# Kernel tuning notes

Measured on AMD Instinct MI355X. Metric: run time of the kernel, lower is better.

Reference implementation:

```python
import jax, jax.numpy as jnp
import numpy as np

B, D, H, T = 16384, 64, 256, 64  # batch, state dim, ODE hidden, time steps
SH = 64  # SAC hidden dim


def setup_inputs() -> dict:
    key = jax.random.key(0)
    ks = jax.random.split(key, 24)
    inv = lambda n: 1.0 / np.sqrt(n)

    def mk(k, shape, scale):
        return jax.random.normal(k, shape, dtype=jnp.float32) * scale

    d = {}
    d["y0"] = jax.random.normal(ks[0], (B, D), dtype=jnp.float32)
    d["t"] = jnp.arange(T, dtype=jnp.float32)
    # pre-sampled standard-normal noise for Normal.rsample at each Euler step
    d["noise"] = jax.random.normal(ks[1], (T - 1, B, D), dtype=jnp.float32)
    # ODEFunc: Linear(D,H)+Tanh, Linear(H,H)+Softplus, Linear(H,D)  (num_layers=2)
    d["ode_W1"] = mk(ks[2], (D, H), inv(D));   d["ode_b1"] = mk(ks[3], (H,), 0.01)
    d["ode_W2"] = mk(ks[4], (H, H), inv(H));   d["ode_b2"] = mk(ks[5], (H,), 0.01)
    d["ode_W3"] = mk(ks[6], (H, D), 0.02);     d["ode_b3"] = mk(ks[7], (D,), 0.01)
    # SAC actor_mean: Linear(D,SH)+ReLU, Linear(SH,SH)+ReLU, Linear(SH,D)+Tanh
    d["am_W1"] = mk(ks[8], (D, SH), inv(D));   d["am_b1"] = mk(ks[9], (SH,), 0.01)
    d["am_W2"] = mk(ks[10], (SH, SH), inv(SH)); d["am_b2"] = mk(ks[11], (SH,), 0.01)
    d["am_W3"] = mk(ks[12], (SH, D), inv(SH)); d["am_b3"] = mk(ks[13], (D,), 0.01)
    # SAC actor_log_std: same shapes, no final tanh
    d["as_W1"] = mk(ks[14], (D, SH), inv(D));  d["as_b1"] = mk(ks[15], (SH,), 0.01)
    d["as_W2"] = mk(ks[16], (SH, SH), inv(SH)); d["as_b2"] = mk(ks[17], (SH,), 0.01)
    d["as_W3"] = mk(ks[18], (SH, D), inv(SH)); d["as_b3"] = mk(ks[19], (D,), 0.01)
    return d


def reference(y0, t, noise,
              ode_W1, ode_b1, ode_W2, ode_b2, ode_W3, ode_b3,
              am_W1, am_b1, am_W2, am_b2, am_W3, am_b3,
              as_W1, as_b1, as_W2, as_b2, as_W3, as_b3):
    dt = t[1] - t[0]  # source computes dt once from first interval

    def ode_func(y):  # ODEFunc.forward (t unused)
        h = jnp.tanh(y @ ode_W1 + ode_b1)
        h = jax.nn.softplus(h @ ode_W2 + ode_b2)
        return h @ ode_W3 + ode_b3

    def clean(x):  # where(isnan|isinf, 0, x)
        return jnp.where(jnp.isfinite(x), x, jnp.zeros_like(x))

    def actor_action(y, eps):  # SAC_Manifold action (critic unused by ODE forward)
        h = jax.nn.relu(y @ am_W1 + am_b1)
        h = jax.nn.relu(h @ am_W2 + am_b2)
        mean = clean(jnp.tanh(h @ am_W3 + am_b3))
        g = jax.nn.relu(y @ as_W1 + as_b1)
        g = jax.nn.relu(g @ as_W2 + as_b2)
        log_std = clean(g @ as_W3 + as_b3)
        std = jax.nn.softplus(log_std)
        x_t = mean + std * eps  # Normal.rsample
        return jnp.tanh(x_t)

    def step(y, eps):
        u = actor_action(y, eps)
        y_new = y + (ode_func(y) - u) * dt
        return y_new, y_new

    _, ys = jax.lax.scan(step, y0, noise)  # [T-1, B, D]
    return jnp.concatenate([y0[None], ys], axis=0)  # [T, B, D]
```

## Files before the change

kernel.cpp:

```cpp
#include <hip/hip_runtime.h>
#include <hip/hip_bf16.h>
#include <math.h>

#define NB 16384
#define DD 64
#define HH 256
#define NSTEP 63
#define RB 32
#define NT 512

#define SYW 68
#define SHW 260

#define O1H 0
#define O1L 16384
#define O2H 32768
#define O2L 98304
#define O3H 163840
#define O3L 180224
#define AM1H 196608
#define AM1L 200704
#define AM2H 204800
#define AM2L 208896
#define AM3H 212992
#define AM3L 217088
#define AS1H 221184
#define AS1L 225280
#define AS2H 229376
#define AS2L 233472
#define AS3H 237568
#define AS3L 241664
#define WB_SHORTS 245760

__device__ unsigned short g_wb[WB_SHORTS];

typedef __attribute__((ext_vector_type(8))) short s8v;
typedef __attribute__((ext_vector_type(4))) float f4v;
typedef __attribute__((ext_vector_type(4))) unsigned int u4v;

#define MFMA(a, b, c) __builtin_amdgcn_mfma_f32_16x16x32_bf16((a), (b), (c), 0, 0, 0)
#define MM3(acc, ah, al, bh, bl)                                 \
    do {                                                         \
        acc = MFMA(ah, bh, acc);                                 \
        acc = MFMA(ah, bl, acc);                                 \
        acc = MFMA(al, bh, acc);                                 \
    } while (0)

__device__ __forceinline__ unsigned short f2b(float x) {
    return __builtin_bit_cast(unsigned short, (__bf16)x);
}
__device__ __forceinline__ float b2f(unsigned short u) {
    return __builtin_bit_cast(float, (unsigned int)u << 16);
}
__device__ __forceinline__ unsigned int packsplit(float x) {
    const unsigned int xb = __builtin_bit_cast(unsigned int, x);
    const unsigned int hb = xb & 0xFFFF0000u;
    const float lof = x - __builtin_bit_cast(float, hb);
    const unsigned int lb = __builtin_bit_cast(unsigned int, lof);
    return __builtin_amdgcn_perm(lb, hb, 0x07060302);
}
__device__ __forceinline__ float fast_tanh(float x) {
    float e = __expf(-2.0f * fabsf(x));
    float r = __fdividef(1.0f - e, 1.0f + e);
    return copysignf(r, x);
}
__device__ __forceinline__ float fast_softplus(float x) {
    return fmaxf(x, 0.0f) + __logf(1.0f + __expf(-fabsf(x)));
}
__device__ __forceinline__ float clean_f(float x) { return isfinite(x) ? x : 0.0f; }
__device__ __forceinline__ f4v splat4(float b) { f4v v = {b, b, b, b}; return v; }

__device__ __forceinline__ void ldsPK(const unsigned int* p, s8v* hi, s8v* lo) {
    const u4v q0 = *(const u4v*)p;
    const u4v q1 = *(const u4v*)(p + 4);
    union { unsigned int u[4]; s8v v; } H, L;
    H.u[0] = __builtin_amdgcn_perm(q0[1], q0[0], 0x05040100);
    L.u[0] = __builtin_amdgcn_perm(q0[1], q0[0], 0x07060302);
    H.u[1] = __builtin_amdgcn_perm(q0[3], q0[2], 0x05040100);
    L.u[1] = __builtin_amdgcn_perm(q0[3], q0[2], 0x07060302);
    H.u[2] = __builtin_amdgcn_perm(q1[1], q1[0], 0x05040100);
    L.u[2] = __builtin_amdgcn_perm(q1[1], q1[0], 0x07060302);
    H.u[3] = __builtin_amdgcn_perm(q1[3], q1[2], 0x05040100);
    L.u[3] = __builtin_amdgcn_perm(q1[3], q1[2], 0x07060302);
    *hi = H.v; *lo = L.v;
}

__device__ __forceinline__ void gld16(const unsigned short* g, unsigned int* l) {
    __builtin_amdgcn_global_load_lds(
        (const __attribute__((address_space(1))) void*)(g),
        (__attribute__((address_space(3))) void*)(l), 16, 0, 0);
}

__device__ __forceinline__ s8v ldw(const unsigned int* wb, int j, int l) {
    return *(const s8v*)((const unsigned short*)wb + j * 512 + l * 8);
}

template <int C>
__device__ __forceinline__ void stage_chunk(unsigned int* dst, int w, int l) {
#pragma unroll
    for (int i = 0; i < 4; ++i) {
        const int j = w * 4 + i;
        int src;
        if constexpr (C == 0)
            src = 384 + ((j >> 4) * 48) + (((j >> 3) & 1) * 8) + (j & 7);
        else if constexpr (C == 1)
            src = 400 + ((j >> 4) * 48) + (((j >> 3) & 1) * 8) + (j & 7);
        else if constexpr (C == 2)
            src = 416 + ((j >> 4) * 48) + (((j >> 3) & 1) * 8) + (j & 7);
        else if constexpr (C == 3)
            src = (j & 15) * 2 + ((j >> 4) * 32);
        else if constexpr (C == 4)
            src = (j & 15) * 2 + 1 + ((j >> 4) * 32);
        else if constexpr (C >= 5 && C <= 12)
            src = 64 + ((j >> 4) * 128) + ((j & 15) * 8) + (C - 5);
        else if constexpr (C == 13)
            src = 320 + (((j >> 2) & 1) * 32) + ((j & 3) * 8) + (j >> 3);
        else
            src = 320 + (((j >> 2) & 1) * 32) + ((j & 3) * 8) + (j >> 3) + 4;
        gld16(g_wb + (size_t)src * 512 + l * 8, dst + j * 256);
    }
}

__global__ void prep_kernel(const float* __restrict__ W, int K, int N,
                            int hi_off, int lo_off) {
    const int l = threadIdx.x;
    const int kcN = K >> 5;
    const int nt = blockIdx.x / kcN;
    const int kc = blockIdx.x % kcN;
    const int col = nt * 16 + (l & 15);
    const int k0 = kc * 32 + ((l >> 4) << 3);
    const size_t base = ((size_t)(nt * kcN + kc) * 64 + l) * 8;
#pragma unroll
    for (int b = 0; b < 8; ++b) {
        float wv = W[(size_t)(k0 + b) * N + col];
        unsigned short h = f2b(wv);
        g_wb[hi_off + base + b] = h;
        g_wb[lo_off + base + b] = f2b(wv - b2f(h));
    }
}

#define SWAP_WB() do { unsigned int* _t = wc; wc = wn_; wn_ = _t; } while (0)

extern "C" __global__ void __launch_bounds__(NT)
ode_sac_kernel(const float* __restrict__ y0,
               const float* __restrict__ tarr,
               const float* __restrict__ noise,
               const float* __restrict__ ob1, const float* __restrict__ ob2,
               const float* __restrict__ ob3,
               const float* __restrict__ amb1, const float* __restrict__ amb2,
               const float* __restrict__ amb3,
               const float* __restrict__ asb1, const float* __restrict__ asb2,
               const float* __restrict__ asb3,
               float* __restrict__ out) {
    __shared__ __align__(16) unsigned int y_pk[RB * SYW];
    __shared__ __align__(16) unsigned int h1_pk[RB * SHW];
    __shared__ __align__(16) unsigned int h2_pk[RB * SHW];
    __shared__ __align__(16) unsigned int wbA[8192];
    __shared__ __align__(16) unsigned int wbB[8192];
    unsigned int* a1m = h1_pk;
    unsigned int* a1s = h1_pk + RB * SYW;
    unsigned int* a2m = h2_pk;
    unsigned int* a2s = h2_pk + RB * SYW;

    const int tid = threadIdx.x;
    const int w  = tid >> 6;
    const int l  = tid & 63;
    const int lm = l & 15;
    const int lg = l >> 4;
    const int wm = w >> 2;
    const int wn = w & 3;
    const int row0 = blockIdx.x * RB;
    const int cN = wn * 16 + lm;

    const float dt = tarr[1] - tarr[0];

    const float b_am1 = amb1[cN], b_am2 = amb2[cN], b_am3 = amb3[cN];
    const float b_as1 = asb1[cN], b_as2 = asb2[cN], b_as3 = asb3[cN];
    const float b_o3  = ob3[cN];
    const float b_o2a = ob2[(w * 2) * 16 + lm];
    const float b_o2b = ob2[(w * 2 + 1) * 16 + lm];
    float b_o1v[4];
#pragma unroll
    for (int nt = 0; nt < 4; ++nt) b_o1v[nt] = ob1[wn * 64 + nt * 16 + lm];

    stage_chunk<0>(wbA, w, l);
    float ysr[4];
#pragma unroll
    for (int r = 0; r < 4; ++r) {
        const int row = wm * 16 + lg * 4 + r;
        const float v = y0[(size_t)(row0 + row) * DD + cN];
        ysr[r] = v;
        y_pk[row * SYW + cN] = packsplit(v);
        __builtin_nontemporal_store(v, &out[(size_t)(row0 + row) * DD + cN]);
    }
    __syncthreads();
    unsigned int* wc = wbA;
    unsigned int* wn_ = wbB;

    for (int t = 0; t < NSTEP; ++t) {
        float u[4], ep[4];
        f4v accB[4];
        f4v acc4[2][2];
        f4v f3;

        stage_chunk<1>(wn_, w, l);
#pragma unroll
        for (int r = 0; r < 4; ++r) {
            const int row = wm * 16 + lg * 4 + r;
            ep[r] = __builtin_nontemporal_load(
                &noise[(size_t)t * NB * DD + (size_t)(row0 + row) * DD + cN]);
        }
        {
            f4v am = splat4(b_am1), as_ = splat4(b_as1);
#pragma unroll
            for (int kc = 0; kc < 2; ++kc) {
                s8v yh, yl;
                ldsPK(&y_pk[(wm * 16 + lm) * SYW + kc * 32 + lg * 8], &yh, &yl);
                MM3(am, yh, yl, ldw(wc, 2 * wn + kc, l), ldw(wc, 8 + 2 * wn + kc, l));
                MM3(as_, yh, yl, ldw(wc, 16 + 2 * wn + kc, l), ldw(wc, 24 + 2 * wn + kc, l));
            }
#pragma unroll
            for (int r = 0; r < 4; ++r) {
                const int row = wm * 16 + lg * 4 + r;
                a1m[row * SYW + cN] = packsplit(fmaxf(am[r], 0.0f));
                a1s[row * SYW + cN] = packsplit(fmaxf(as_[r], 0.0f));
            }
        }
        __syncthreads(); SWAP_WB();

        stage_chunk<2>(wn_, w, l);
        {
            f4v am = splat4(b_am2), as_ = splat4(b_as2);
#pragma unroll
            for (int kc = 0; kc < 2; ++kc) {
                const int k0 = kc * 32 + lg * 8;
                s8v mh, ml, sh, sl;
                ldsPK(&a1m[(wm * 16 + lm) * SYW + k0], &mh, &ml);
                ldsPK(&a1s[(wm * 16 + lm) * SYW + k0], &sh, &sl);
                MM3(am, mh, ml, ldw(wc, 2 * wn + kc, l), ldw(wc, 8 + 2 * wn + kc, l));
                MM3(as_, sh, sl, ldw(wc, 16 + 2 * wn + kc, l), ldw(wc, 24 + 2 * wn + kc, l));
            }
#pragma unroll
            for (int r = 0; r < 4; ++r) {
                const int row = wm * 16 + lg * 4 + r;
                a2m[row * SYW + cN] = packsplit(fmaxf(am[r], 0.0f));
                a2s[row * SYW + cN] = packsplit(fmaxf(as_[r], 0.0f));
            }
        }
        __syncthreads(); SWAP_WB();

        stage_chunk<3>(wn_, w, l);
        {
            f4v m3 = splat4(b_am3), s3 = splat4(b_as3);
#pragma unroll
            for (int kc = 0; kc < 2; ++kc) {
                const int k0 = kc * 32 + lg * 8;
                s8v mh, ml, sh, sl;
                ldsPK(&a2m[(wm * 16 + lm) * SYW + k0], &mh, &ml);
                ldsPK(&a2s[(wm * 16 + lm) * SYW + k0], &sh, &sl);
                MM3(m3, mh, ml, ldw(wc, 2 * wn + kc, l), ldw(wc, 8 + 2 * wn + kc, l));
                MM3(s3, sh, sl, ldw(wc, 16 + 2 * wn + kc, l), ldw(wc, 24 + 2 * wn + kc, l));
            }
#pragma unroll
            for (int r = 0; r < 4; ++r) {
                const float mean = clean_f(fast_tanh(m3[r]));
                const float ls   = clean_f(s3[r]);
                const float sd   = fast_softplus(ls);
                u[r] = fast_tanh(mean + sd * ep[r]);
            }
        }
        __syncthreads(); SWAP_WB();

        stage_chunk<4>(wn_, w, l);
        {
#pragma unroll
            for (int nt = 0; nt < 4; ++nt) accB[nt] = splat4(b_o1v[nt]);
            s8v yh, yl;
            ldsPK(&y_pk[(wm * 16 + lm) * SYW + 0 * 32 + lg * 8], &yh, &yl);
#pragma unroll
            for (int nt = 0; nt < 4; ++nt)
                MM3(accB[nt], yh, yl, ldw(wc, 4 * wn + nt, l), ldw(wc, 16 + 4 * wn + nt, l));
        }
        __syncthreads(); SWAP_WB();

        stage_chunk<5>(wn_, w, l);
        {
            s8v yh, yl;
            ldsPK(&y_pk[(wm * 16 + lm) * SYW + 1 * 32 + lg * 8], &yh, &yl);
#pragma unroll
            for (int nt = 0; nt < 4; ++nt)
                MM3(accB[nt], yh, yl, ldw(wc, 4 * wn + nt, l), ldw(wc, 16 + 4 * wn + nt, l));
#pragma unroll
            for (int nt = 0; nt < 4; ++nt)
#pragma unroll
                for (int r = 0; r < 4; ++r) {
                    const int row = wm * 16 + lg * 4 + r;
                    const int col = wn * 64 + nt * 16 + lm;
                    h1_pk[row * SHW + col] = packsplit(fast_tanh(accB[nt][r]));
                }
        }
        __syncthreads(); SWAP_WB();

        acc4[0][0] = splat4(b_o2a); acc4[0][1] = splat4(b_o2b);
        acc4[1][0] = splat4(b_o2a); acc4[1][1] = splat4(b_o2b);
#define P4_BODY(Q)                                                            \
        {                                                                     \
            const int k0 = (Q) * 32 + lg * 8;                                 \
            s8v a0h, a0l, a1h_, a1l_;                                         \
            ldsPK(&h1_pk[(0 * 16 + lm) * SHW + k0], &a0h, &a0l);              \
            ldsPK(&h1_pk[(1 * 16 + lm) * SHW + k0], &a1h_, &a1l_);            \
            const s8v bh0 = ldw(wc, 2 * w, l),     bl0 = ldw(wc, 16 + 2 * w, l); \
            const s8v bh1 = ldw(wc, 2 * w + 1, l), bl1 = ldw(wc, 17 + 2 * w, l); \
            MM3(acc4[0][0], a0h, a0l, bh0, bl0);                              \
            MM3(acc4[0][1], a0h, a0l, bh1, bl1);                              \
            MM3(acc4[1][0], a1h_, a1l_, bh0, bl0);                            \
            MM3(acc4[1][1], a1h_, a1l_, bh1, bl1);                            \
        }
        stage_chunk<6>(wn_, w, l);  P4_BODY(0) __syncthreads(); SWAP_WB();
        stage_chunk<7>(wn_, w, l);  P4_BODY(1) __syncthreads(); SWAP_WB();
        stage_chunk<8>(wn_, w, l);  P4_BODY(2) __syncthreads(); SWAP_WB();
        stage_chunk<9>(wn_, w, l);  P4_BODY(3) __syncthreads(); SWAP_WB();
        stage_chunk<10>(wn_, w, l); P4_BODY(4) __syncthreads(); SWAP_WB();
        stage_chunk<11>(wn_, w, l); P4_BODY(5) __syncthreads(); SWAP_WB();
        stage_chunk<12>(wn_, w, l); P4_BODY(6) __syncthreads(); SWAP_WB();
        stage_chunk<13>(wn_, w, l);
        P4_BODY(7)
        {
#pragma unroll
            for (int mt = 0; mt < 2; ++mt)
#pragma unroll
                for (int ct = 0; ct < 2; ++ct)
#pragma unroll
                    for (int r = 0; r < 4; ++r) {
                        const int row = mt * 16 + lg * 4 + r;
                        const int col = (w * 2 + ct) * 16 + lm;
                        h2_pk[row * SHW + col] = packsplit(fast_softplus(acc4[mt][ct][r]));
                    }
        }
        __syncthreads(); SWAP_WB();

        stage_chunk<14>(wn_, w, l);
        f3 = splat4(b_o3);
#pragma unroll
        for (int kc = 0; kc < 4; ++kc) {
            s8v ah, al;
            ldsPK(&h2_pk[(wm * 16 + lm) * SHW + kc * 32 + lg * 8], &ah, &al);
            MM3(f3, ah, al, ldw(wc, kc * 8 + wn, l), ldw(wc, kc * 8 + 4 + wn, l));
        }
        __syncthreads(); SWAP_WB();

        stage_chunk<0>(wn_, w, l);
#pragma unroll
        for (int kc = 4; kc < 8; ++kc) {
            s8v ah, al;
            ldsPK(&h2_pk[(wm * 16 + lm) * SHW + kc * 32 + lg * 8], &ah, &al);
            MM3(f3, ah, al, ldw(wc, (kc - 4) * 8 + wn, l), ldw(wc, (kc - 4) * 8 + 4 + wn, l));
        }
#pragma unroll
        for (int r = 0; r < 4; ++r) {
            const int row = wm * 16 + lg * 4 + r;
            const float yn = ysr[r] + (f3[r] - u[r]) * dt;
            ysr[r] = yn;
            y_pk[row * SYW + cN] = packsplit(yn);
            __builtin_nontemporal_store(yn,
                &out[(size_t)(t + 1) * NB * DD + (size_t)(row0 + row) * DD + cN]);
        }
        __syncthreads(); SWAP_WB();
    }
}

extern "C" void kernel_launch(void* const* d_in, const int* in_sizes, int n_in,
                              void* d_out, int out_size, void* d_ws, size_t ws_size,
                              hipStream_t stream) {
    const float* y0    = (const float*)d_in[0];
    const float* tarr  = (const float*)d_in[1];
    const float* noise = (const float*)d_in[2];
    const float* oW1 = (const float*)d_in[3];  const float* ob1 = (const float*)d_in[4];
    const float* oW2 = (const float*)d_in[5];  const float* ob2 = (const float*)d_in[6];
    const float* oW3 = (const float*)d_in[7];  const float* ob3 = (const float*)d_in[8];
    const float* amW1 = (const float*)d_in[9];  const float* amb1 = (const float*)d_in[10];
    const float* amW2 = (const float*)d_in[11]; const float* amb2 = (const float*)d_in[12];
    const float* amW3 = (const float*)d_in[13]; const float* amb3 = (const float*)d_in[14];
    const float* asW1 = (const float*)d_in[15]; const float* asb1 = (const float*)d_in[16];
    const float* asW2 = (const float*)d_in[17]; const float* asb2 = (const float*)d_in[18];
    const float* asW3 = (const float*)d_in[19]; const float* asb3 = (const float*)d_in[20];
    float* out = (float*)d_out;

    hipLaunchKernelGGL(prep_kernel, dim3(16 * 2), dim3(64), 0, stream, oW1, 64, 256, O1H, O1L);
    hipLaunchKernelGGL(prep_kernel, dim3(16 * 8), dim3(64), 0, stream, oW2, 256, 256, O2H, O2L);
    hipLaunchKernelGGL(prep_kernel, dim3(4 * 8),  dim3(64), 0, stream, oW3, 256, 64, O3H, O3L);
    hipLaunchKernelGGL(prep_kernel, dim3(4 * 2),  dim3(64), 0, stream, amW1, 64, 64, AM1H, AM1L);
    hipLaunchKernelGGL(prep_kernel, dim3(4 * 2),  dim3(64), 0, stream, amW2, 64, 64, AM2H, AM2L);
    hipLaunchKernelGGL(prep_kernel, dim3(4 * 2),  dim3(64), 0, stream, amW3, 64, 64, AM3H, AM3L);
    hipLaunchKernelGGL(prep_kernel, dim3(4 * 2),  dim3(64), 0, stream, asW1, 64, 64, AS1H, AS1L);
    hipLaunchKernelGGL(prep_kernel, dim3(4 * 2),  dim3(64), 0, stream, asW2, 64, 64, AS2H, AS2L);
    hipLaunchKernelGGL(prep_kernel, dim3(4 * 2),  dim3(64), 0, stream, asW3, 64, 64, AS3H, AS3L);

    hipLaunchKernelGGL(ode_sac_kernel, dim3(NB / RB), dim3(NT), 0, stream,
                       y0, tarr, noise,
                       ob1, ob2, ob3, amb1, amb2, amb3, asb1, asb2, asb3,
                       out);
}
```

Measured before the change: 1.581 ms.

## Double block to 1024 threads, splitting actor branches and ODE tiles across warp halves

Doubles threads per block from 512 to 1024. The two halves of the block now compute the actor-mean and actor-log_std branches separately and split the ODE layer tiles, each wave handling fewer MFMA tiles. The final layer is divided so one half computes part of the split-precision product while the other adds a partial sum through shared memory. The aim is more parallel waves to hide latency, at the cost of an extra barrier and shared-memory exchange per step and higher register pressure per thread.

```diff
diff --git a/kernel.cpp b/kernel.cpp
--- a/kernel.cpp
+++ b/kernel.cpp
@@ -7,7 +7,7 @@
 #define HH 256
 #define NSTEP 63
 #define RB 32
-#define NT 512
+#define NT 1024
 
 #define SYW 68
 #define SHW 260
@@ -90,7 +90,6 @@
         (const __attribute__((address_space(1))) void*)(g),
         (__attribute__((address_space(3))) void*)(l), 16, 0, 0);
 }
-
 __device__ __forceinline__ s8v ldw(const unsigned int* wb, int j, int l) {
     return *(const s8v*)((const unsigned short*)wb + j * 512 + l * 8);
 }
@@ -98,8 +97,8 @@
 template <int C>
 __device__ __forceinline__ void stage_chunk(unsigned int* dst, int w, int l) {
 #pragma unroll
-    for (int i = 0; i < 4; ++i) {
-        const int j = w * 4 + i;
+    for (int i = 0; i < 2; ++i) {
+        const int j = w * 2 + i;
         int src;
         if constexpr (C == 0)
             src = 384 + ((j >> 4) * 48) + (((j >> 3) & 1) * 8) + (j & 7);
@@ -114,9 +113,9 @@
         else if constexpr (C >= 5 && C <= 12)
             src = 64 + ((j >> 4) * 128) + ((j & 15) * 8) + (C - 5);
         else if constexpr (C == 13)
-            src = 320 + (((j >> 2) & 1) * 32) + ((j & 3) * 8) + (j >> 3);
+            src = 320 + j;
         else
-            src = 320 + (((j >> 2) & 1) * 32) + ((j & 3) * 8) + (j >> 3) + 4;
+            src = 352 + j;
         gld16(g_wb + (size_t)src * 512 + l * 8, dst + j * 256);
     }
 }
@@ -161,160 +160,179 @@
     unsigned int* a1s = h1_pk + RB * SYW;
     unsigned int* a2m = h2_pk;
     unsigned int* a2s = h2_pk + RB * SYW;
+    float* sdep_s = (float*)(h1_pk + 2 * RB * SYW);
+    float* f3b_s  = (float*)h1_pk;
 
     const int tid = threadIdx.x;
     const int w  = tid >> 6;
     const int l  = tid & 63;
     const int lm = l & 15;
     const int lg = l >> 4;
-    const int wm = w >> 2;
-    const int wn = w & 3;
+    const int hw = w >> 3;
+    const int w7 = w & 7;
+    const int wm = w7 >> 2;
+    const int wn = w7 & 3;
+    const int cB = w & 7;
     const int row0 = blockIdx.x * RB;
     const int cN = wn * 16 + lm;
 
     const float dt = tarr[1] - tarr[0];
 
-    const float b_am1 = amb1[cN], b_am2 = amb2[cN], b_am3 = amb3[cN];
-    const float b_as1 = asb1[cN], b_as2 = asb2[cN], b_as3 = asb3[cN];
-    const float b_o3  = ob3[cN];
-    const float b_o2a = ob2[(w * 2) * 16 + lm];
-    const float b_o2b = ob2[(w * 2 + 1) * 16 + lm];
-    float b_o1v[4];
-#pragma unroll
-    for (int nt = 0; nt < 4; ++nt) b_o1v[nt] = ob1[wn * 64 + nt * 16 + lm];
+    const float b1  = hw ? asb1[cN] : amb1[cN];
+    const float b2  = hw ? asb2[cN] : amb2[cN];
+    const float b3a = hw ? asb3[cN] : amb3[cN];
+    const float b_o3 = ob3[cN];
+    const float b_o2 = ob2[w * 16 + lm];
+    float b_o1v[2];
+#pragma unroll
+    for (int i = 0; i < 2; ++i) b_o1v[i] = ob1[(2 * cB + i) * 16 + lm];
+
+    unsigned int* a1dst = hw ? a1s : a1m;
+    unsigned int* a2dst = hw ? a2s : a2m;
 
     stage_chunk<0>(wbA, w, l);
     float ysr[4];
-#pragma unroll
-    for (int r = 0; r < 4; ++r) {
-        const int row = wm * 16 + lg * 4 + r;
-        const float v = y0[(size_t)(row0 + row) * DD + cN];
-        ysr[r] = v;
-        y_pk[row * SYW + cN] = packsplit(v);
-        __builtin_nontemporal_store(v, &out[(size_t)(row0 + row) * DD + cN]);
+    if (hw == 0) {
+#pragma unroll
+        for (int r = 0; r < 4; ++r) {
+            const int row = wm * 16 + lg * 4 + r;
+            const float v = y0[(size_t)(row0 + row) * DD + cN];
+            ysr[r] = v;
+            y_pk[row * SYW + cN] = packsplit(v);
+            __builtin_nontemporal_store(v, &out[(size_t)(row0 + row) * DD + cN]);
+        }
     }
     __syncthreads();
     unsigned int* wc = wbA;
     unsigned int* wn_ = wbB;
 
     for (int t = 0; t < NSTEP; ++t) {
-        float u[4], ep[4];
-        f4v accB[4];
-        f4v acc4[2][2];
-        f4v f3;
+        float u[4], mean[4], ep[4];
+        f4v accB[2], acc4[2], f3;
 
         stage_chunk<1>(wn_, w, l);
-#pragma unroll
-        for (int r = 0; r < 4; ++r) {
-            const int row = wm * 16 + lg * 4 + r;
-            ep[r] = __builtin_nontemporal_load(
-                &noise[(size_t)t * NB * DD + (size_t)(row0 + row) * DD + cN]);
-        }
-        {
-            f4v am = splat4(b_am1), as_ = splat4(b_as1);
+        if (hw) {
+#pragma unroll
+            for (int r = 0; r < 4; ++r) {
+                const int row = wm * 16 + lg * 4 + r;
+                ep[r] = __builtin_nontemporal_load(
+                    &noise[(size_t)t * NB * DD + (size_t)(row0 + row) * DD + cN]);
+            }
+        }
+        {
+            f4v a = splat4(b1);
+            const int base = hw * 16;
 #pragma unroll
             for (int kc = 0; kc < 2; ++kc) {
                 s8v yh, yl;
                 ldsPK(&y_pk[(wm * 16 + lm) * SYW + kc * 32 + lg * 8], &yh, &yl);
-                MM3(am, yh, yl, ldw(wc, 2 * wn + kc, l), ldw(wc, 8 + 2 * wn + kc, l));
-                MM3(as_, yh, yl, ldw(wc, 16 + 2 * wn + kc, l), ldw(wc, 24 + 2 * wn + kc, l));
+                MM3(a, yh, yl, ldw(wc, base + 2 * wn + kc, l),
+                    ldw(wc, base + 8 + 2 * wn + kc, l));
             }
 #pragma unroll
             for (int r = 0; r < 4; ++r) {
                 const int row = wm * 16 + lg * 4 + r;
-                a1m[row * SYW + cN] = packsplit(fmaxf(am[r], 0.0f));
-                a1s[row * SYW + cN] = packsplit(fmaxf(as_[r], 0.0f));
+                a1dst[row * SYW + cN] = packsplit(fmaxf(a[r], 0.0f));
             }
         }
         __syncthreads(); SWAP_WB();
 
         stage_chunk<2>(wn_, w, l);
         {
-            f4v am = splat4(b_am2), as_ = splat4(b_as2);
+            f4v a = splat4(b2);
+            const int base = hw * 16;
 #pragma unroll
             for (int kc = 0; kc < 2; ++kc) {
-                const int k0 = kc * 32 + lg * 8;
-                s8v mh, ml, sh, sl;
-                ldsPK(&a1m[(wm * 16 + lm) * SYW + k0], &mh, &ml);
-                ldsPK(&a1s[(wm * 16 + lm) * SYW + k0], &sh, &sl);
-                MM3(am, mh, ml, ldw(wc, 2 * wn + kc, l), ldw(wc, 8 + 2 * wn + kc, l));
-                MM3(as_, sh, sl, ldw(wc, 16 + 2 * wn + kc, l), ldw(wc, 24 + 2 * wn + kc, l));
+                s8v ah, al;
+                ldsPK(&a1dst[(wm * 16 + lm) * SYW + kc * 32 + lg * 8], &ah, &al);
+                MM3(a, ah, al, ldw(wc, base + 2 * wn + kc, l),
+                    ldw(wc, base + 8 + 2 * wn + kc, l));
             }
 #pragma unroll
             for (int r = 0; r < 4; ++r) {
                 const int row = wm * 16 + lg * 4 + r;
-                a2m[row * SYW + cN] = packsplit(fmaxf(am[r], 0.0f));
-                a2s[row * SYW + cN] = packsplit(fmaxf(as_[r], 0.0f));
+                a2dst[row * SYW + cN] = packsplit(fmaxf(a[r], 0.0f));
             }
         }
         __syncthreads(); SWAP_WB();
 
         stage_chunk<3>(wn_, w, l);
         {
-            f4v m3 = splat4(b_am3), s3 = splat4(b_as3);
+            f4v a = splat4(b3a);
+            const int base = hw * 16;
 #pragma unroll
             for (int kc = 0; kc < 2; ++kc) {
-                const int k0 = kc * 32 + lg * 8;
-                s8v mh, ml, sh, sl;
-                ldsPK(&a2m[(wm * 16 + lm) * SYW + k0], &mh, &ml);
-                ldsPK(&a2s[(wm * 16 + lm) * SYW + k0], &sh, &sl);
-                MM3(m3, mh, ml, ldw(wc, 2 * wn + kc, l), ldw(wc, 8 + 2 * wn + kc, l));
-                MM3(s3, sh, sl, ldw(wc, 16 + 2 * wn + kc, l), ldw(wc, 24 + 2 * wn + kc, l));
-            }
-#pragma unroll
-            for (int r = 0; r < 4; ++r) {
-                const float mean = clean_f(fast_tanh(m3[r]));
-                const float ls   = clean_f(s3[r]);
-                const float sd   = fast_softplus(ls);
-                u[r] = fast_tanh(mean + sd * ep[r]);
-            }
-        }
-        __syncthreads(); SWAP_WB();
-
-        stage_chunk<4>(wn_, w, l);
-        {
-#pragma unroll
-            for (int nt = 0; nt < 4; ++nt) accB[nt] = splat4(b_o1v[nt]);
-            s8v yh, yl;
-            ldsPK(&y_pk[(wm * 16 + lm) * SYW + 0 * 32 + lg * 8], &yh, &yl);
-#pragma unroll
-            for (int nt = 0; nt < 4; ++nt)
-                MM3(accB[nt], yh, yl, ldw(wc, 4 * wn + nt, l), ldw(wc, 16 + 4 * wn + nt, l));
-        }
-        __syncthreads(); SWAP_WB();
-
-        stage_chunk<5>(wn_, w, l);
-        {
-            s8v yh, yl;
-            ldsPK(&y_pk[(wm * 16 + lm) * SYW + 1 * 32 + lg * 8], &yh, &yl);
-#pragma unroll
-            for (int nt = 0; nt < 4; ++nt)
-                MM3(accB[nt], yh, yl, ldw(wc, 4 * wn + nt, l), ldw(wc, 16 + 4 * wn + nt, l));
-#pragma unroll
-            for (int nt = 0; nt < 4; ++nt)
+                s8v ah, al;
+                ldsPK(&a2dst[(wm * 16 + lm) * SYW + kc * 32 + lg * 8], &ah, &al);
+                MM3(a, ah, al, ldw(wc, base + 2 * wn + kc, l),
+                    ldw(wc, base + 8 + 2 * wn + kc, l));
+            }
+            if (hw) {
 #pragma unroll
                 for (int r = 0; r < 4; ++r) {
                     const int row = wm * 16 + lg * 4 + r;
-                    const int col = wn * 64 + nt * 16 + lm;
-                    h1_pk[row * SHW + col] = packsplit(fast_tanh(accB[nt][r]));
+                    const float ls = clean_f(a[r]);
+                    sdep_s[row * 68 + cN] = fast_softplus(ls) * ep[r];
                 }
-        }
-        __syncthreads(); SWAP_WB();
-
-        acc4[0][0] = splat4(b_o2a); acc4[0][1] = splat4(b_o2b);
-        acc4[1][0] = splat4(b_o2a); acc4[1][1] = splat4(b_o2b);
+            } else {
+#pragma unroll
+                for (int r = 0; r < 4; ++r) mean[r] = clean_f(fast_tanh(a[r]));
+            }
+        }
+        __syncthreads(); SWAP_WB();
+
+        stage_chunk<4>(wn_, w, l);
+        if (hw == 0) {
+#pragma unroll
+            for (int r = 0; r < 4; ++r) {
+                const int row = wm * 16 + lg * 4 + r;
+                u[r] = fast_tanh(mean[r] + sdep_s[row * 68 + cN]);
+            }
+        }
+        {
+#pragma unroll
+            for (int i = 0; i < 2; ++i) accB[i] = splat4(b_o1v[i]);
+            s8v yh, yl;
+            ldsPK(&y_pk[(hw * 16 + lm) * SYW + lg * 8], &yh, &yl);
+#pragma unroll
+            for (int i = 0; i < 2; ++i) {
+                const int nt = 2 * cB + i;
+                MM3(accB[i], yh, yl, ldw(wc, nt, l), ldw(wc, 16 + nt, l));
+            }
+        }
+        __syncthreads(); SWAP_WB();
+
+        stage_chunk<5>(wn_, w, l);
+        {
+            s8v yh, yl;
+            ldsPK(&y_pk[(hw * 16 + lm) * SYW + 32 + lg * 8], &yh, &yl);
+#pragma unroll
+            for (int i = 0; i < 2; ++i) {
+                const int nt = 2 * cB + i;
+                MM3(accB[i], yh, yl, ldw(wc, nt, l), ldw(wc, 16 + nt, l));
+            }
+#pragma unroll
+            for (int i = 0; i < 2; ++i)
+#pragma unroll
+                for (int r = 0; r < 4; ++r) {
+                    const int row = hw * 16 + lg * 4 + r;
+                    const int col = (2 * cB + i) * 16 + lm;
+                    h1_pk[row * SHW + col] = packsplit(fast_tanh(accB[i][r]));
+                }
+        }
+        __syncthreads(); SWAP_WB();
+
+        acc4[0] = splat4(b_o2);
+        acc4[1] = splat4(b_o2);
 #define P4_BODY(Q)                                                            \
         {                                                                     \
             const int k0 = (Q) * 32 + lg * 8;                                 \
             s8v a0h, a0l, a1h_, a1l_;                                         \
-            ldsPK(&h1_pk[(0 * 16 + lm) * SHW + k0], &a0h, &a0l);              \
-            ldsPK(&h1_pk[(1 * 16 + lm) * SHW + k0], &a1h_, &a1l_);            \
-            const s8v bh0 = ldw(wc, 2 * w, l),     bl0 = ldw(wc, 16 + 2 * w, l); \
-            const s8v bh1 = ldw(wc, 2 * w + 1, l), bl1 = ldw(wc, 17 + 2 * w, l); \
-            MM3(acc4[0][0], a0h, a0l, bh0, bl0);                              \
-            MM3(acc4[0][1], a0h, a0l, bh1, bl1);                              \
-            MM3(acc4[1][0], a1h_, a1l_, bh0, bl0);                            \
-            MM3(acc4[1][1], a1h_, a1l_, bh1, bl1);                            \
+            ldsPK(&h1_pk[(lm) * SHW + k0], &a0h, &a0l);                       \
+            ldsPK(&h1_pk[(16 + lm) * SHW + k0], &a1h_, &a1l_);                \
+            const s8v bh = ldw(wc, w, l), bl = ldw(wc, 16 + w, l);            \
+            MM3(acc4[0], a0h, a0l, bh, bl);                                   \
+            MM3(acc4[1], a1h_, a1l_, bh, bl);                                 \
         }
         stage_chunk<6>(wn_, w, l);  P4_BODY(0) __syncthreads(); SWAP_WB();
         stage_chunk<7>(wn_, w, l);  P4_BODY(1) __syncthreads(); SWAP_WB();
@@ -329,43 +347,56 @@
 #pragma unroll
             for (int mt = 0; mt < 2; ++mt)
 #pragma unroll
-                for (int ct = 0; ct < 2; ++ct)
-#pragma unroll
-                    for (int r = 0; r < 4; ++r) {
-                        const int row = mt * 16 + lg * 4 + r;
-                        const int col = (w * 2 + ct) * 16 + lm;
-                        h2_pk[row * SHW + col] = packsplit(fast_softplus(acc4[mt][ct][r]));
-                    }
+                for (int r = 0; r < 4; ++r) {
+                    const int row = mt * 16 + lg * 4 + r;
+                    const int col = w * 16 + lm;
+                    h2_pk[row * SHW + col] = packsplit(fast_softplus(acc4[mt][r]));
+                }
         }
         __syncthreads(); SWAP_WB();
 
         stage_chunk<14>(wn_, w, l);
-        f3 = splat4(b_o3);
-#pragma unroll
-        for (int kc = 0; kc < 4; ++kc) {
-            s8v ah, al;
-            ldsPK(&h2_pk[(wm * 16 + lm) * SHW + kc * 32 + lg * 8], &ah, &al);
-            MM3(f3, ah, al, ldw(wc, kc * 8 + wn, l), ldw(wc, kc * 8 + 4 + wn, l));
+        if (hw == 0) {
+            f3 = splat4(b_o3);
+#pragma unroll
+            for (int kc = 0; kc < 8; ++kc) {
+                s8v ah, al;
+                ldsPK(&h2_pk[(wm * 16 + lm) * SHW + kc * 32 + lg * 8], &ah, &al);
+                const s8v bh = ldw(wc, wn * 8 + kc, l);
+                f3 = MFMA(ah, bh, f3);
+                f3 = MFMA(al, bh, f3);
+            }
         }
         __syncthreads(); SWAP_WB();
 
         stage_chunk<0>(wn_, w, l);
-#pragma unroll
-        for (int kc = 4; kc < 8; ++kc) {
-            s8v ah, al;
-            ldsPK(&h2_pk[(wm * 16 + lm) * SHW + kc * 32 + lg * 8], &ah, &al);
-            MM3(f3, ah, al, ldw(wc, (kc - 4) * 8 + wn, l), ldw(wc, (kc - 4) * 8 + 4 + wn, l));
-        }
-#pragma unroll
-        for (int r = 0; r < 4; ++r) {
-            const int row = wm * 16 + lg * 4 + r;
-            const float yn = ysr[r] + (f3[r] - u[r]) * dt;
-            ysr[r] = yn;
-            y_pk[row * SYW + cN] = packsplit(yn);
-            __builtin_nontemporal_store(yn,
-                &out[(size_t)(t + 1) * NB * DD + (size_t)(row0 + row) * DD + cN]);
-        }
-        __syncthreads(); SWAP_WB();
+        if (hw) {
+            f4v fb = {0.0f, 0.0f, 0.0f, 0.0f};
+#pragma unroll
+            for (int kc = 0; kc < 8; ++kc) {
+                s8v ah, al;
+                ldsPK(&h2_pk[(wm * 16 + lm) * SHW + kc * 32 + lg * 8], &ah, &al);
+                fb = MFMA(ah, ldw(wc, wn * 8 + kc, l), fb);
+            }
+#pragma unroll
+            for (int r = 0; r < 4; ++r)
+                f3b_s[(wm * 16 + lg * 4 + r) * 68 + cN] = fb[r];
+        }
+        __syncthreads(); SWAP_WB();
+
+        if (hw == 0) {
+#pragma unroll
+            for (int r = 0; r < 4; ++r) {
+                const int row = wm * 16 + lg * 4 + r;
+                const float f = f3[r] + f3b_s[row * 68 + cN];
+                const float yn = ysr[r] + (f - u[r]) * dt;
+                ysr[r] = yn;
+                y_pk[row * SYW + cN] = packsplit(yn);
+                __builtin_nontemporal_store(yn,
+                    &out[(size_t)(t + 1) * NB * DD + (size_t)(row0 + row) * DD + cN]);
+            }
+        }
+        __syncthreads();
     }
 }
 
```

New measurement: 2.889 ms. 82.8% more time.
